# Kernel tuning notes

Hardware: AMD Instinct MI355X
Metric: run time of the kernel (lower is better)

Reference implementation:

```python
import jax, jax.numpy as jnp
import numpy as np

NUM_EXPERTS = 8
TOP_K = 2
D_MODEL = 1024
D_MLP = 3584
BATCH, POS = 2, 2048


def setup_inputs() -> dict:
    key = jax.random.key(0)
    ks = jax.random.split(key, 5)
    scale = 0.02
    x = jax.random.normal(ks[0], (BATCH, POS, D_MODEL), dtype=jnp.float32)
    W_gate = jax.random.normal(ks[1], (NUM_EXPERTS, D_MODEL), dtype=jnp.float32) * scale
    W1 = jax.random.normal(ks[2], (NUM_EXPERTS, D_MLP, D_MODEL), dtype=jnp.float32) * scale
    W3 = jax.random.normal(ks[3], (NUM_EXPERTS, D_MLP, D_MODEL), dtype=jnp.float32) * scale
    W2 = jax.random.normal(ks[4], (NUM_EXPERTS, D_MODEL, D_MLP), dtype=jnp.float32) * scale
    return {"x": x, "W_gate": W_gate, "W1": W1, "W3": W3, "W2": W2}


def reference(x, W_gate, W1, W3, W2):
    batch, pos, d_model = x.shape
    xt = x.reshape(-1, d_model)                      # [T, d]
    T = xt.shape[0]

    # --- top-2 softmax gating ---
    gate_logits = xt @ W_gate.T                      # [T, E]
    weights = jax.nn.softmax(gate_logits.astype(jnp.float32), axis=-1)
    top_w, top_i = jax.lax.top_k(weights, TOP_K)     # [T, k]
    top_w = top_w / jnp.sum(top_w, axis=-1, keepdims=True)
    top_w = top_w.astype(gate_logits.dtype)

    # dense combine weights: zero for non-selected experts  [T, E]
    combine = jnp.zeros((T, NUM_EXPERTS), dtype=xt.dtype)
    combine = combine.at[jnp.arange(T)[:, None], top_i].set(top_w)

    # --- per-expert SwiGLU MLP, computed dense over all tokens ---
    h1 = jnp.einsum('td,efd->etf', xt, W1)           # [E, T, ffn]
    h3 = jnp.einsum('td,efd->etf', xt, W3)           # [E, T, ffn]
    h = jax.nn.silu(h1) * h3                         # [E, T, ffn]
    expert_out = jnp.einsum('etf,edf->etd', h, W2)   # [E, T, d]

    # --- weighted combine ---
    out = jnp.einsum('etd,te->td', expert_out, combine)  # [T, d]
    return out.reshape(batch, pos, d_model)
```

## Files before the change

### kernel.cpp

```cpp
#include <hip/hip_runtime.h>
#include <hip/hip_bf16.h>
#include <math.h>


#define NUM_EXPERTS 8
#define TOPK 2
#define D_MODEL 1024
#define D_MLP 3584
#define T_TOKENS 4096
#define NSLOT (T_TOKENS * TOPK)
#define SLOT_CAP 9216

#define BM 128
#define BN 128
#define BK 32
#define LDT 40

typedef __attribute__((ext_vector_type(8))) short bf16x8;
typedef __attribute__((ext_vector_type(4))) float f32x4;

#define WS_SMALL 147456
#define H_BYTES ((size_t)SLOT_CAP * D_MLP * 2)
#define XB_OFF (WS_SMALL + H_BYTES)
#define XB_BYTES ((size_t)T_TOKENS * D_MODEL * 2)
#define W1B_OFF (XB_OFF + XB_BYTES)
#define W13_BYTES ((size_t)NUM_EXPERTS * (size_t)D_MLP * D_MODEL * 2)
#define W3B_OFF (W1B_OFF + W13_BYTES)
#define WS_FULL (W3B_OFF + W13_BYTES)
#define W2B_OFF WS_FULL
#define WS_BIG (W2B_OFF + W13_BYTES)
#define WS_NEEDED_OLD (WS_SMALL + H_BYTES)

#define NW8 (NUM_EXPERTS * D_MLP * D_MODEL / 8)

__device__ inline unsigned short f32_to_bf16(float f) {
  union { float f; unsigned int u; } v; v.f = f;
  unsigned int u = v.u;
  unsigned int r = (u + 0x7FFFu + ((u >> 16) & 1u)) >> 16;
  return (unsigned short)r;
}

__device__ inline bf16x8 pack8(float4 a, float4 b) {
  bf16x8 v;
  v[0] = (short)f32_to_bf16(a.x); v[1] = (short)f32_to_bf16(a.y);
  v[2] = (short)f32_to_bf16(a.z); v[3] = (short)f32_to_bf16(a.w);
  v[4] = (short)f32_to_bf16(b.x); v[5] = (short)f32_to_bf16(b.y);
  v[6] = (short)f32_to_bf16(b.z); v[7] = (short)f32_to_bf16(b.w);
  return v;
}

__device__ __forceinline__ void gload16(const void* g, void* l) {
  __builtin_amdgcn_global_load_lds(
      (__attribute__((address_space(1))) void*)g,
      (__attribute__((address_space(3))) void*)l, 16, 0, 0);
}

__global__ void zero_kernel(float4* __restrict__ p, int n4) {
  int i = blockIdx.x * blockDim.x + threadIdx.x;
  if (i < n4) p[i] = make_float4(0.f, 0.f, 0.f, 0.f);
}

__global__ __launch_bounds__(256) void cvt_kernel(const float* __restrict__ src,
                                                  unsigned short* __restrict__ dst,
                                                  int n8) {
  int i = blockIdx.x * blockDim.x + threadIdx.x;
  const int stride = gridDim.x * blockDim.x;
  for (; i < n8; i += stride) {
    const float4* s = (const float4*)(src + (size_t)i * 8);
    float4 a = s[0], b = s[1];
    *(bf16x8*)(dst + (size_t)i * 8) = pack8(a, b);
  }
}

__global__ __launch_bounds__(64) void gate_kernel(const float* __restrict__ x,
                            const float* __restrict__ Wg,
                            int* __restrict__ top_idx,
                            float* __restrict__ top_w,
                            unsigned short* __restrict__ Xb) {
  const int t = blockIdx.x;
  const int lane = threadIdx.x;
  const float* xr = x + (size_t)t * D_MODEL;

  float xs[16];
#pragma unroll
  for (int i = 0; i < 16; ++i) xs[i] = xr[lane + i * 64];

  if (Xb) {
    const float4* xr4 = (const float4*)(xr + lane * 16);
    float4 a0 = xr4[0], a1 = xr4[1], a2 = xr4[2], a3 = xr4[3];
    unsigned short* xbrow = Xb + (size_t)t * D_MODEL + lane * 16;
    *(bf16x8*)(xbrow) = pack8(a0, a1);
    *(bf16x8*)(xbrow + 8) = pack8(a2, a3);
  }

  float logits[NUM_EXPERTS];
#pragma unroll
  for (int e = 0; e < NUM_EXPERTS; ++e) {
    const float* wr = Wg + (size_t)e * D_MODEL;
    float s = 0.f;
#pragma unroll
    for (int i = 0; i < 16; ++i) s += xs[i] * wr[lane + i * 64];
    for (int o = 32; o > 0; o >>= 1) s += __shfl_down(s, o);
    logits[e] = s;
  }

  if (lane == 0) {
    int i0 = 0;
#pragma unroll
    for (int e = 1; e < NUM_EXPERTS; ++e)
      if (logits[e] > logits[i0]) i0 = e;
    int i1 = -1;
#pragma unroll
    for (int e = 0; e < NUM_EXPERTS; ++e) {
      if (e == i0) continue;
      if (i1 < 0 || logits[e] > logits[i1]) i1 = e;
    }
    float w0 = 1.0f / (1.0f + expf(logits[i1] - logits[i0]));
    top_idx[2 * t] = i0; top_idx[2 * t + 1] = i1;
    top_w[2 * t] = w0;   top_w[2 * t + 1] = 1.0f - w0;
  }
}

__global__ __launch_bounds__(256) void route_cvt_kernel(
    int* __restrict__ top_idx,
    const float* __restrict__ top_w,
    int* __restrict__ hdr,
    int* __restrict__ slot_token,
    float* __restrict__ slot_weight,
    const float* __restrict__ W1,
    const float* __restrict__ W3,
    const float* __restrict__ W2,
    unsigned short* __restrict__ W1b,
    unsigned short* __restrict__ W3b,
    unsigned short* __restrict__ W2b) {
  const int tid = threadIdx.x;
  if (blockIdx.x != 0) {
    const int wid = blockIdx.x - 1;
    const int stride = (gridDim.x - 1) * 256;
    for (int i = wid * 256 + tid; i < NW8; i += stride) {
      const float4* s = (const float4*)(W1 + (size_t)i * 8);
      float4 a = s[0], b = s[1];
      *(bf16x8*)(W1b + (size_t)i * 8) = pack8(a, b);
    }
    for (int i = wid * 256 + tid; i < NW8; i += stride) {
      const float4* s = (const float4*)(W3 + (size_t)i * 8);
      float4 a = s[0], b = s[1];
      *(bf16x8*)(W3b + (size_t)i * 8) = pack8(a, b);
    }
    if (W2) {
      for (int i = wid * 256 + tid; i < NW8; i += stride) {
        const float4* s = (const float4*)(W2 + (size_t)i * 8);
        float4 a = s[0], b = s[1];
        *(bf16x8*)(W2b + (size_t)i * 8) = pack8(a, b);
      }
    }
    return;
  }
  __shared__ int cnt[NUM_EXPERTS];
  __shared__ int off[NUM_EXPERTS];
  __shared__ int cur[NUM_EXPERTS];
  if (tid < NUM_EXPERTS) cnt[tid] = 0;
  __syncthreads();
  for (int k = tid; k < NSLOT; k += 256) atomicAdd(&cnt[top_idx[k]], 1);
  __syncthreads();
  if (tid == 0) {
    int o = 0;
    for (int e = 0; e < NUM_EXPERTS; ++e) {
      off[e] = o;
      int p = (cnt[e] + BM - 1) & ~(BM - 1);
      hdr[e] = cnt[e];
      hdr[8 + e] = o;
      hdr[16 + e] = p;
      o += p;
    }
  }
  __syncthreads();
  if (tid < NUM_EXPERTS) cur[tid] = off[tid];
  for (int i = tid; i < SLOT_CAP; i += 256) { slot_token[i] = 0; slot_weight[i] = 0.0f; }
  __syncthreads();
  for (int k = tid; k < NSLOT; k += 256) {
    int e = top_idx[k];
    int p = atomicAdd(&cur[e], 1);
    slot_token[p] = k >> 1;
    slot_weight[p] = top_w[k];
    top_idx[k] = p;
  }
}

__global__ __launch_bounds__(256) void gemm1_p(
    const unsigned short* __restrict__ Xb,
    const unsigned short* __restrict__ W1b,
    const unsigned short* __restrict__ W3b,
    const int* __restrict__ hdr,
    const int* __restrict__ slot_token,
    unsigned short* __restrict__ H) {
  const int e = blockIdx.z;
  const int pad_cnt = hdr[16 + e];
  const int m0 = blockIdx.y * BM;
  if (m0 >= pad_cnt) return;
  const int base = hdr[8 + e];
  const int n0 = blockIdx.x * BN;

  __shared__ unsigned short As[2][BM * BK];
  __shared__ unsigned short B1s[2][BN * BK];
  __shared__ unsigned short B3s[2][BN * BK];

  const int tid = threadIdx.x;
  const int lane = tid & 63;
  const int wave = tid >> 6;
  const int wm = (wave >> 1) * 64;
  const int wn = (wave & 1) * 64;
  const int l15 = lane & 15;
  const int quad = lane >> 4;

  const int r0 = tid >> 2;
  const int cc = (tid & 3) * 8;
  const int tokA0 = slot_token[base + m0 + r0];
  const int tokA1 = slot_token[base + m0 + 64 + r0];
  const unsigned short* gA0 = Xb + (size_t)tokA0 * D_MODEL + cc;
  const unsigned short* gA1 = Xb + (size_t)tokA1 * D_MODEL + cc;
  const unsigned short* gB1_0 = W1b + ((size_t)e * D_MLP + n0 + r0) * D_MODEL + cc;
  const unsigned short* gB1_1 = gB1_0 + (size_t)64 * D_MODEL;
  const unsigned short* gB3_0 = W3b + ((size_t)e * D_MLP + n0 + r0) * D_MODEL + cc;
  const unsigned short* gB3_1 = gB3_0 + (size_t)64 * D_MODEL;
  const int wb = wave * 512;

  const f32x4 fzero = {0.f, 0.f, 0.f, 0.f};
  f32x4 acc1[4][4], acc3[4][4];
#pragma unroll
  for (int i = 0; i < 4; ++i)
#pragma unroll
    for (int j = 0; j < 4; ++j) { acc1[i][j] = fzero; acc3[i][j] = fzero; }

#define NT1 (D_MODEL / BK)
  gload16(gA0, &As[0][wb]);
  gload16(gA1, &As[0][2048 + wb]);
  gload16(gB1_0, &B1s[0][wb]);
  gload16(gB1_1, &B1s[0][2048 + wb]);
  gload16(gB3_0, &B3s[0][wb]);
  gload16(gB3_1, &B3s[0][2048 + wb]);

#pragma unroll
  for (int t = 0; t < NT1; ++t) {
    const int p = t & 1;
    if (t + 1 < NT1) {
      const int q = (t + 1) & 1;
      const int k1 = (t + 1) * BK;
      gload16(gA0 + k1, &As[q][wb]);
      gload16(gA1 + k1, &As[q][2048 + wb]);
      gload16(gB1_0 + k1, &B1s[q][wb]);
      gload16(gB1_1 + k1, &B1s[q][2048 + wb]);
      gload16(gB3_0 + k1, &B3s[q][wb]);
      gload16(gB3_1 + k1, &B3s[q][2048 + wb]);
      asm volatile("s_waitcnt vmcnt(6)" ::: "memory");
    } else {
      asm volatile("s_waitcnt vmcnt(0)" ::: "memory");
    }
    __builtin_amdgcn_s_barrier();
    asm volatile("" ::: "memory");

    bf16x8 af[4], b1f[4], b3f[4];
#pragma unroll
    for (int i = 0; i < 4; ++i)
      af[i] = *(const bf16x8*)(&As[p][(wm + i * 16 + l15) * BK + quad * 8]);
#pragma unroll
    for (int j = 0; j < 4; ++j) {
      b1f[j] = *(const bf16x8*)(&B1s[p][(wn + j * 16 + l15) * BK + quad * 8]);
      b3f[j] = *(const bf16x8*)(&B3s[p][(wn + j * 16 + l15) * BK + quad * 8]);
    }
#pragma unroll
    for (int i = 0; i < 4; ++i)
#pragma unroll
      for (int j = 0; j < 4; ++j) {
        acc1[i][j] = __builtin_amdgcn_mfma_f32_16x16x32_bf16(af[i], b1f[j], acc1[i][j], 0, 0, 0);
        acc3[i][j] = __builtin_amdgcn_mfma_f32_16x16x32_bf16(af[i], b3f[j], acc3[i][j], 0, 0, 0);
      }
    asm volatile("" ::: "memory");
    __builtin_amdgcn_s_barrier();
  }

  const size_t hbase = (size_t)(base + m0);
#pragma unroll
  for (int i = 0; i < 4; ++i) {
    const int mrow = wm + i * 16 + quad * 4;
#pragma unroll
    for (int r = 0; r < 4; ++r) {
      unsigned short* hrow = H + (hbase + mrow + r) * D_MLP + n0;
#pragma unroll
      for (int j = 0; j < 4; ++j) {
        float h1 = acc1[i][j][r];
        float h3 = acc3[i][j][r];
        float s = h1 / (1.0f + __expf(-h1));
        hrow[wn + j * 16 + l15] = f32_to_bf16(s * h3);
      }
    }
  }
}

__global__ __launch_bounds__(256) void gemm2_p(
    const unsigned short* __restrict__ H,
    const unsigned short* __restrict__ W2b,
    const int* __restrict__ hdr,
    float* __restrict__ Y) {
  const int e = blockIdx.z;
  const int pad_cnt = hdr[16 + e];
  const int m0 = blockIdx.y * BM;
  if (m0 >= pad_cnt) return;
  const int base = hdr[8 + e];
  const int n0 = blockIdx.x * BN;

  __shared__ unsigned short As[2][BM * BK];
  __shared__ unsigned short Bs[2][BN * BK];

  const int tid = threadIdx.x;
  const int lane = tid & 63;
  const int wave = tid >> 6;
  const int wm = (wave >> 1) * 64;
  const int wn = (wave & 1) * 64;
  const int l15 = lane & 15;
  const int quad = lane >> 4;

  const int r0 = tid >> 2;
  const int cc = (tid & 3) * 8;
  const unsigned short* gA0 = H + (size_t)(base + m0 + r0) * D_MLP + cc;
  const unsigned short* gA1 = gA0 + (size_t)64 * D_MLP;
  const unsigned short* gB0 = W2b + ((size_t)e * D_MODEL + n0 + r0) * D_MLP + cc;
  const unsigned short* gB1 = gB0 + (size_t)64 * D_MLP;
  const int wb = wave * 512;

  const f32x4 fzero = {0.f, 0.f, 0.f, 0.f};
  f32x4 acc[4][4];
#pragma unroll
  for (int i = 0; i < 4; ++i)
#pragma unroll
    for (int j = 0; j < 4; ++j) acc[i][j] = fzero;

#define NT2 (D_MLP / BK)
  gload16(gA0, &As[0][wb]);
  gload16(gA1, &As[0][2048 + wb]);
  gload16(gB0, &Bs[0][wb]);
  gload16(gB1, &Bs[0][2048 + wb]);

#pragma unroll 2
  for (int t = 0; t < NT2; ++t) {
    const int p = t & 1;
    if (t + 1 < NT2) {
      const int q = (t + 1) & 1;
      const int k1 = (t + 1) * BK;
      gload16(gA0 + k1, &As[q][wb]);
      gload16(gA1 + k1, &As[q][2048 + wb]);
      gload16(gB0 + k1, &Bs[q][wb]);
      gload16(gB1 + k1, &Bs[q][2048 + wb]);
      asm volatile("s_waitcnt vmcnt(4)" ::: "memory");
    } else {
      asm volatile("s_waitcnt vmcnt(0)" ::: "memory");
    }
    __builtin_amdgcn_s_barrier();
    asm volatile("" ::: "memory");

    bf16x8 af[4], bf[4];
#pragma unroll
    for (int i = 0; i < 4; ++i)
      af[i] = *(const bf16x8*)(&As[p][(wm + i * 16 + l15) * BK + quad * 8]);
#pragma unroll
    for (int j = 0; j < 4; ++j)
      bf[j] = *(const bf16x8*)(&Bs[p][(wn + j * 16 + l15) * BK + quad * 8]);
#pragma unroll
    for (int i = 0; i < 4; ++i)
#pragma unroll
      for (int j = 0; j < 4; ++j)
        acc[i][j] = __builtin_amdgcn_mfma_f32_16x16x32_bf16(af[i], bf[j], acc[i][j], 0, 0, 0);
    asm volatile("" ::: "memory");
    __builtin_amdgcn_s_barrier();
  }

#pragma unroll
  for (int i = 0; i < 4; ++i) {
    const int mrow = wm + i * 16 + quad * 4;
#pragma unroll
    for (int r = 0; r < 4; ++r) {
      float* yrow = Y + (size_t)(base + m0 + mrow + r) * D_MODEL + n0;
#pragma unroll
      for (int j = 0; j < 4; ++j)
        yrow[wn + j * 16 + l15] = acc[i][j][r];
    }
  }
}

__global__ __launch_bounds__(256) void combine_kernel(
    const float* __restrict__ Y,
    const int* __restrict__ slot_of,
    const float* __restrict__ top_w,
    float* __restrict__ out) {
  const int t = blockIdx.x;
  const int c = threadIdx.x;
  const int p0 = slot_of[2 * t], p1 = slot_of[2 * t + 1];
  const float w0 = top_w[2 * t], w1 = top_w[2 * t + 1];
  const float4 y0 = ((const float4*)(Y + (size_t)p0 * D_MODEL))[c];
  const float4 y1 = ((const float4*)(Y + (size_t)p1 * D_MODEL))[c];
  float4 o;
  o.x = w0 * y0.x + w1 * y1.x;
  o.y = w0 * y0.y + w1 * y1.y;
  o.z = w0 * y0.z + w1 * y1.z;
  o.w = w0 * y0.w + w1 * y1.w;
  ((float4*)(out + (size_t)t * D_MODEL))[c] = o;
}


__global__ __launch_bounds__(256) void gemm1_kernel(const float* __restrict__ x,
                             const float* __restrict__ W1,
                             const float* __restrict__ W3,
                             const int* __restrict__ hdr,
                             const int* __restrict__ slot_token,
                             unsigned short* __restrict__ H) {
  const int e = blockIdx.z;
  const int pad_cnt = hdr[16 + e];
  const int m0 = blockIdx.y * BM;
  if (m0 >= pad_cnt) return;
  const int base = hdr[8 + e];
  const int n0 = blockIdx.x * BN;

  __shared__ unsigned short As[BM * LDT];
  __shared__ unsigned short B1s[BN * LDT];
  __shared__ unsigned short B3s[BN * LDT];

  const int tid = threadIdx.x;
  const int lane = tid & 63;
  const int wave = tid >> 6;
  const int wm = (wave >> 1) * 64;
  const int wn = (wave & 1) * 64;
  const int l15 = lane & 15;
  const int quad = lane >> 4;

  const int sr = tid >> 1;
  const int sc = (tid & 1) * 16;
  const float* arow = x + (size_t)slot_token[base + m0 + sr] * D_MODEL + sc;
  const float* b1row = W1 + ((size_t)e * D_MLP + n0 + sr) * D_MODEL + sc;
  const float* b3row = W3 + ((size_t)e * D_MLP + n0 + sr) * D_MODEL + sc;

  const f32x4 fzero = {0.f, 0.f, 0.f, 0.f};
  f32x4 acc1[4][4], acc3[4][4];
#pragma unroll
  for (int i = 0; i < 4; ++i)
#pragma unroll
    for (int j = 0; j < 4; ++j) { acc1[i][j] = fzero; acc3[i][j] = fzero; }

  for (int k0 = 0; k0 < D_MODEL; k0 += BK) {
    const float4* ap = (const float4*)(arow + k0);
    const float4* b1p = (const float4*)(b1row + k0);
    const float4* b3p = (const float4*)(b3row + k0);
    float4 a0 = ap[0], a1 = ap[1], a2 = ap[2], a3 = ap[3];
    float4 c0 = b1p[0], c1 = b1p[1], c2 = b1p[2], c3 = b1p[3];
    float4 d0 = b3p[0], d1 = b3p[1], d2 = b3p[2], d3 = b3p[3];
    __syncthreads();
    *(bf16x8*)(&As[sr * LDT + sc]) = pack8(a0, a1);
    *(bf16x8*)(&As[sr * LDT + sc + 8]) = pack8(a2, a3);
    *(bf16x8*)(&B1s[sr * LDT + sc]) = pack8(c0, c1);
    *(bf16x8*)(&B1s[sr * LDT + sc + 8]) = pack8(c2, c3);
    *(bf16x8*)(&B3s[sr * LDT + sc]) = pack8(d0, d1);
    *(bf16x8*)(&B3s[sr * LDT + sc + 8]) = pack8(d2, d3);
    __syncthreads();

    bf16x8 a_frag[4], b1_frag[4], b3_frag[4];
#pragma unroll
    for (int i = 0; i < 4; ++i)
      a_frag[i] = *(const bf16x8*)(&As[(wm + i * 16 + l15) * LDT + quad * 8]);
#pragma unroll
    for (int j = 0; j < 4; ++j) {
      b1_frag[j] = *(const bf16x8*)(&B1s[(wn + j * 16 + l15) * LDT + quad * 8]);
      b3_frag[j] = *(const bf16x8*)(&B3s[(wn + j * 16 + l15) * LDT + quad * 8]);
    }
#pragma unroll
    for (int i = 0; i < 4; ++i)
#pragma unroll
      for (int j = 0; j < 4; ++j) {
        acc1[i][j] = __builtin_amdgcn_mfma_f32_16x16x32_bf16(a_frag[i], b1_frag[j], acc1[i][j], 0, 0, 0);
        acc3[i][j] = __builtin_amdgcn_mfma_f32_16x16x32_bf16(a_frag[i], b3_frag[j], acc3[i][j], 0, 0, 0);
      }
  }

  const size_t hbase = (size_t)(base + m0);
#pragma unroll
  for (int i = 0; i < 4; ++i) {
    const int mrow = wm + i * 16 + quad * 4;
#pragma unroll
    for (int r = 0; r < 4; ++r) {
      unsigned short* hrow = H + (hbase + mrow + r) * D_MLP + n0;
#pragma unroll
      for (int j = 0; j < 4; ++j) {
        float h1 = acc1[i][j][r];
        float h3 = acc3[i][j][r];
        float s = h1 / (1.0f + __expf(-h1));
        hrow[wn + j * 16 + l15] = f32_to_bf16(s * h3);
      }
    }
  }
}

__global__ __launch_bounds__(256) void gemm2_kernel(const unsigned short* __restrict__ H,
                             const float* __restrict__ W2,
                             const int* __restrict__ hdr,
                             const int* __restrict__ slot_token,
                             const float* __restrict__ slot_weight,
                             float* __restrict__ out) {
  const int e = blockIdx.z;
  const int pad_cnt = hdr[16 + e];
  const int m0 = blockIdx.y * BM;
  if (m0 >= pad_cnt) return;
  const int base = hdr[8 + e];
  const int n0 = blockIdx.x * BN;

  __shared__ unsigned short As[BM * LDT];
  __shared__ unsigned short Bs[BN * LDT];

  const int tid = threadIdx.x;
  const int lane = tid & 63;
  const int wave = tid >> 6;
  const int wm = (wave >> 1) * 64;
  const int wn = (wave & 1) * 64;
  const int l15 = lane & 15;
  const int quad = lane >> 4;

  const int sr = tid >> 1;
  const int sc = (tid & 1) * 16;
  const unsigned short* arow = H + (size_t)(base + m0 + sr) * D_MLP + sc;
  const float* brow = W2 + ((size_t)e * D_MODEL + n0 + sr) * D_MLP + sc;

  const f32x4 fzero = {0.f, 0.f, 0.f, 0.f};
  f32x4 acc[4][4];
#pragma unroll
  for (int i = 0; i < 4; ++i)
#pragma unroll
    for (int j = 0; j < 4; ++j) acc[i][j] = fzero;

  for (int k0 = 0; k0 < D_MLP; k0 += BK) {
    const uint4* ap = (const uint4*)(arow + k0);
    uint4 a0 = ap[0], a1 = ap[1];
    const float4* bp = (const float4*)(brow + k0);
    float4 c0 = bp[0], c1 = bp[1], c2 = bp[2], c3 = bp[3];
    __syncthreads();
    *(uint4*)(&As[sr * LDT + sc]) = a0;
    *(uint4*)(&As[sr * LDT + sc + 8]) = a1;
    *(bf16x8*)(&Bs[sr * LDT + sc]) = pack8(c0, c1);
    *(bf16x8*)(&Bs[sr * LDT + sc + 8]) = pack8(c2, c3);
    __syncthreads();

    bf16x8 a_frag[4], b_frag[4];
#pragma unroll
    for (int i = 0; i < 4; ++i)
      a_frag[i] = *(const bf16x8*)(&As[(wm + i * 16 + l15) * LDT + quad * 8]);
#pragma unroll
    for (int j = 0; j < 4; ++j)
      b_frag[j] = *(const bf16x8*)(&Bs[(wn + j * 16 + l15) * LDT + quad * 8]);
#pragma unroll
    for (int i = 0; i < 4; ++i)
#pragma unroll
      for (int j = 0; j < 4; ++j)
        acc[i][j] = __builtin_amdgcn_mfma_f32_16x16x32_bf16(a_frag[i], b_frag[j], acc[i][j], 0, 0, 0);
  }

#pragma unroll
  for (int i = 0; i < 4; ++i) {
    const int mrow = wm + i * 16 + quad * 4;
#pragma unroll
    for (int r = 0; r < 4; ++r) {
      const int srow = base + m0 + mrow + r;
      const float w = slot_weight[srow];
      if (w != 0.0f) {
        const int tok = slot_token[srow];
        float* orow = out + (size_t)tok * D_MODEL + n0;
#pragma unroll
        for (int j = 0; j < 4; ++j)
          atomicAdd(&orow[wn + j * 16 + l15], acc[i][j][r] * w);
      }
    }
  }
}

extern "C" void kernel_launch(void* const* d_in, const int* in_sizes, int n_in,
                              void* d_out, int out_size, void* d_ws, size_t ws_size,
                              hipStream_t stream) {
  const float* x  = (const float*)d_in[0];
  const float* Wg = (const float*)d_in[1];
  const float* W1 = (const float*)d_in[2];
  const float* W3 = (const float*)d_in[3];
  const float* W2 = (const float*)d_in[4];
  float* out = (float*)d_out;

  if (ws_size < WS_NEEDED_OLD) return;

  char* ws = (char*)d_ws;
  int*   top_idx     = (int*)(ws);
  float* top_w       = (float*)(ws + 32768);
  int*   hdr         = (int*)(ws + 65536);
  int*   slot_token  = (int*)(ws + 65792);
  float* slot_weight = (float*)(ws + 102656);
  unsigned short* H  = (unsigned short*)(ws + WS_SMALL);

  if (ws_size >= WS_FULL) {
    unsigned short* Xb  = (unsigned short*)(ws + XB_OFF);
    unsigned short* W1b = (unsigned short*)(ws + W1B_OFF);
    unsigned short* W3b = (unsigned short*)(ws + W3B_OFF);
    float* Y = (float*)(ws + W3B_OFF);
    const bool big = (ws_size >= WS_BIG);
    unsigned short* W2b = big ? (unsigned short*)(ws + W2B_OFF)
                              : W1b;

    gate_kernel<<<T_TOKENS, 64, 0, stream>>>(x, Wg, top_idx, top_w, Xb);
    route_cvt_kernel<<<2049, 256, 0, stream>>>(
        top_idx, top_w, hdr, slot_token, slot_weight,
        W1, W3, big ? W2 : nullptr, W1b, W3b, W2b);
    gemm1_p<<<dim3(D_MLP / BN, T_TOKENS / BM, NUM_EXPERTS), 256, 0, stream>>>(
        Xb, W1b, W3b, hdr, slot_token, H);
    if (!big) cvt_kernel<<<2048, 256, 0, stream>>>(W2, W2b, NW8);
    gemm2_p<<<dim3(D_MODEL / BN, T_TOKENS / BM, NUM_EXPERTS), 256, 0, stream>>>(
        H, W2b, hdr, Y);
    combine_kernel<<<T_TOKENS, 256, 0, stream>>>(Y, top_idx, top_w, out);
  } else {
    gate_kernel<<<T_TOKENS, 64, 0, stream>>>(x, Wg, top_idx, top_w, nullptr);
    route_cvt_kernel<<<1, 256, 0, stream>>>(
        top_idx, top_w, hdr, slot_token, slot_weight,
        nullptr, nullptr, nullptr, nullptr, nullptr, nullptr);
    zero_kernel<<<(out_size / 4 + 255) / 256, 256, 0, stream>>>((float4*)d_out, out_size / 4);
    gemm1_kernel<<<dim3(D_MLP / BN, T_TOKENS / BM, NUM_EXPERTS), 256, 0, stream>>>(
        x, W1, W3, hdr, slot_token, H);
    gemm2_kernel<<<dim3(D_MODEL / BN, T_TOKENS / BM, NUM_EXPERTS), 256, 0, stream>>>(
        H, W2, hdr, slot_token, slot_weight, out);
  }
}
```

Baseline: 630.9 us.

## Split gemm2 K dimension in two and sum partials in combine

The second expert GEMM is split along the D_MLP reduction into two halves, each written to its own fp32 partial buffer, which doubles the number of workgroups. The combine kernel then reads both partials and adds them before applying the routing weights. The aim is better CU occupancy for the gemm2 grid, which is small (8 N tiles x M tiles x 8 experts, many of them empty). In exchange, the extra fp32 Y buffer adds write and read traffic, and Y1 reuses the W1b workspace region.

```diff
diff --git a/kernel.cpp b/kernel.cpp
--- a/kernel.cpp
+++ b/kernel.cpp
@@ -301,13 +301,19 @@
     const unsigned short* __restrict__ H,
     const unsigned short* __restrict__ W2b,
     const int* __restrict__ hdr,
-    float* __restrict__ Y) {
-  const int e = blockIdx.z;
+    float* __restrict__ Y0,
+    float* __restrict__ Y1) {
+  const int kparts = gridDim.z >> 3;
+  const int e = blockIdx.z / kparts;
+  const int kh = blockIdx.z - e * kparts;
   const int pad_cnt = hdr[16 + e];
   const int m0 = blockIdx.y * BM;
   if (m0 >= pad_cnt) return;
   const int base = hdr[8 + e];
   const int n0 = blockIdx.x * BN;
+  float* __restrict__ Y = kh ? Y1 : Y0;
+  const int nsteps = (D_MLP / BK) / kparts;
+  const int kbase = kh * nsteps * BK;
 
   __shared__ unsigned short As[2][BM * BK];
   __shared__ unsigned short Bs[2][BN * BK];
@@ -322,9 +328,9 @@
 
   const int r0 = tid >> 2;
   const int cc = (tid & 3) * 8;
-  const unsigned short* gA0 = H + (size_t)(base + m0 + r0) * D_MLP + cc;
+  const unsigned short* gA0 = H + (size_t)(base + m0 + r0) * D_MLP + cc + kbase;
   const unsigned short* gA1 = gA0 + (size_t)64 * D_MLP;
-  const unsigned short* gB0 = W2b + ((size_t)e * D_MODEL + n0 + r0) * D_MLP + cc;
+  const unsigned short* gB0 = W2b + ((size_t)e * D_MODEL + n0 + r0) * D_MLP + cc + kbase;
   const unsigned short* gB1 = gB0 + (size_t)64 * D_MLP;
   const int wb = wave * 512;
 
@@ -335,16 +341,15 @@
 #pragma unroll
     for (int j = 0; j < 4; ++j) acc[i][j] = fzero;
 
-#define NT2 (D_MLP / BK)
   gload16(gA0, &As[0][wb]);
   gload16(gA1, &As[0][2048 + wb]);
   gload16(gB0, &Bs[0][wb]);
   gload16(gB1, &Bs[0][2048 + wb]);
 
 #pragma unroll 2
-  for (int t = 0; t < NT2; ++t) {
+  for (int t = 0; t < nsteps; ++t) {
     const int p = t & 1;
-    if (t + 1 < NT2) {
+    if (t + 1 < nsteps) {
       const int q = (t + 1) & 1;
       const int k1 = (t + 1) * BK;
       gload16(gA0 + k1, &As[q][wb]);
@@ -388,16 +393,24 @@
 }
 
 __global__ __launch_bounds__(256) void combine_kernel(
-    const float* __restrict__ Y,
+    const float* __restrict__ Y0,
+    const float* __restrict__ Y1,
     const int* __restrict__ slot_of,
     const float* __restrict__ top_w,
-    float* __restrict__ out) {
+    float* __restrict__ out,
+    int two) {
   const int t = blockIdx.x;
   const int c = threadIdx.x;
   const int p0 = slot_of[2 * t], p1 = slot_of[2 * t + 1];
   const float w0 = top_w[2 * t], w1 = top_w[2 * t + 1];
-  const float4 y0 = ((const float4*)(Y + (size_t)p0 * D_MODEL))[c];
-  const float4 y1 = ((const float4*)(Y + (size_t)p1 * D_MODEL))[c];
+  float4 y0 = ((const float4*)(Y0 + (size_t)p0 * D_MODEL))[c];
+  float4 y1 = ((const float4*)(Y0 + (size_t)p1 * D_MODEL))[c];
+  if (two) {
+    const float4 z0 = ((const float4*)(Y1 + (size_t)p0 * D_MODEL))[c];
+    const float4 z1 = ((const float4*)(Y1 + (size_t)p1 * D_MODEL))[c];
+    y0.x += z0.x; y0.y += z0.y; y0.z += z0.z; y0.w += z0.w;
+    y1.x += z1.x; y1.y += z1.y; y1.z += z1.z; y1.w += z1.w;
+  }
   float4 o;
   o.x = w0 * y0.x + w1 * y1.x;
   o.y = w0 * y0.y + w1 * y1.y;
@@ -601,7 +614,8 @@
     unsigned short* Xb  = (unsigned short*)(ws + XB_OFF);
     unsigned short* W1b = (unsigned short*)(ws + W1B_OFF);
     unsigned short* W3b = (unsigned short*)(ws + W3B_OFF);
-    float* Y = (float*)(ws + W3B_OFF);
+    float* Y0 = (float*)(ws + W3B_OFF);
+    float* Y1 = (float*)(ws + W1B_OFF);
     const bool big = (ws_size >= WS_BIG);
     unsigned short* W2b = big ? (unsigned short*)(ws + W2B_OFF)
                               : W1b;
@@ -613,9 +627,15 @@
     gemm1_p<<<dim3(D_MLP / BN, T_TOKENS / BM, NUM_EXPERTS), 256, 0, stream>>>(
         Xb, W1b, W3b, hdr, slot_token, H);
     if (!big) cvt_kernel<<<2048, 256, 0, stream>>>(W2, W2b, NW8);
-    gemm2_p<<<dim3(D_MODEL / BN, T_TOKENS / BM, NUM_EXPERTS), 256, 0, stream>>>(
-        H, W2b, hdr, Y);
-    combine_kernel<<<T_TOKENS, 256, 0, stream>>>(Y, top_idx, top_w, out);
+    if (big) {
+      gemm2_p<<<dim3(D_MODEL / BN, T_TOKENS / BM, NUM_EXPERTS * 2), 256, 0, stream>>>(
+          H, W2b, hdr, Y0, Y1);
+      combine_kernel<<<T_TOKENS, 256, 0, stream>>>(Y0, Y1, top_idx, top_w, out, 1);
+    } else {
+      gemm2_p<<<dim3(D_MODEL / BN, T_TOKENS / BM, NUM_EXPERTS), 256, 0, stream>>>(
+          H, W2b, hdr, Y0, Y0);
+      combine_kernel<<<T_TOKENS, 256, 0, stream>>>(Y0, Y0, top_idx, top_w, out, 0);
+    }
   } else {
     gate_kernel<<<T_TOKENS, 64, 0, stream>>>(x, Wg, top_idx, top_w, nullptr);
     route_cvt_kernel<<<1, 256, 0, stream>>>(
```

Measured after the change: 637.5 us. About the same (+1.0%).
